# Kernel optimization log

Hardware: AMD Instinct MI355X
Metric: run time of the kernel (lower is better)

Reference implementation:

```python
import jax, jax.numpy as jnp
import numpy as np

N = 100000
E = 1600000
D_IN = 128
D_OUT = 128


def setup_inputs() -> dict:
    key = jax.random.key(0)
    ks = jax.random.split(key, 6)
    seq = jax.random.normal(ks[0], (N, D_IN), dtype=jnp.float32)
    edge_src = jax.random.randint(ks[1], (E,), 0, N, dtype=jnp.int32)
    edge_dst = jax.random.randint(ks[2], (E,), 0, N, dtype=jnp.int32)
    adj_vals = jax.random.uniform(ks[3], (E,), dtype=jnp.float32)
    # xavier_uniform for [out, in] -> stored as [in, out] for x @ W
    lim = float(np.sqrt(6.0 / (D_IN + D_OUT)))
    w_fc = jax.random.uniform(ks[4], (D_IN, D_OUT), jnp.float32, -lim, lim)
    w_proj = jax.random.uniform(ks[5], (D_IN, D_OUT), jnp.float32, -lim, lim)
    b_proj = jnp.zeros((D_OUT,), jnp.float32)
    bias = jnp.zeros((D_OUT,), jnp.float32)
    return {"seq": seq, "edge_src": edge_src, "edge_dst": edge_dst,
            "adj_vals": adj_vals, "w_fc": w_fc, "w_proj": w_proj,
            "b_proj": b_proj, "bias": bias}


def reference(seq, edge_src, edge_dst, adj_vals, w_fc, w_proj, b_proj, bias):
    # h = fc(seq)  (no bias)
    h = seq @ w_fc                                  # [N, D_OUT]
    # spmm(adj, h): out[i] = sum_{e: dst=i} vals[e] * h[src[e]]
    msgs = adj_vals[:, None] * h[edge_src]          # [E, D_OUT]
    agg = jax.ops.segment_sum(msgs, edge_dst, num_segments=N)
    # bias add + residual proj(seq) add + tanh
    out = jnp.tanh(agg + bias + seq @ w_proj + b_proj)
    return out
```

## Files before the change

### kernel.cpp

```cpp
#include <hip/hip_runtime.h>
#include <math.h>


typedef __attribute__((ext_vector_type(8))) short short8;
typedef __attribute__((ext_vector_type(4))) float float4v;
typedef __attribute__((ext_vector_type(2))) _Float16 half2v;

#define PG 256
#define NBMAX 2048

static __device__ __forceinline__ short f2bf(float x) {
    unsigned u = __float_as_uint(x);
    unsigned r = (u + 0x7fffu + ((u >> 16) & 1u)) >> 16;
    return (short)r;
}
static __device__ __forceinline__ float bf2f(short h) {
    return __uint_as_float(((unsigned)(unsigned short)h) << 16);
}

__global__ __launch_bounds__(256)
void wconv_kernel(const float* __restrict__ wa, const float* __restrict__ wb,
                  short* __restrict__ whia, short* __restrict__ wloa,
                  short* __restrict__ whib, short* __restrict__ wlob) {
    const int bb = blockIdx.x;
    const float* w  = (bb < 16) ? wa   : wb;
    short* whi      = (bb < 16) ? whia : whib;
    short* wlo      = (bb < 16) ? wloa : wlob;
    const int i = (bb & 15) * 256 + threadIdx.x;
    const float4 v = ((const float4*)w)[i];
    const int k = i >> 5;
    const int c4 = (i & 31) * 4;
    float xs[4] = {v.x, v.y, v.z, v.w};
    #pragma unroll
    for (int j = 0; j < 4; j++) {
        const short hi = f2bf(xs[j]);
        const short lo = f2bf(xs[j] - bf2f(hi));
        whi[(c4 + j) * 128 + k] = hi;
        wlo[(c4 + j) * 128 + k] = lo;
    }
}

#define KP 136

__global__ __launch_bounds__(256, 2)
void mm_mfma_kernel(const float* __restrict__ seq, const short* __restrict__ whi,
                    const short* __restrict__ wlo,
                    const float* __restrict__ b0p, const float* __restrict__ b1p,
                    float* __restrict__ out, _Float16* __restrict__ out16,
                    int N, int add_bias) {
    __shared__ short wt_hi[128 * KP];
    __shared__ short wt_lo[128 * KP];

    const int tid = threadIdx.x;
    for (int i = tid; i < 2048; i += 256) {
        const int row = i >> 4;
        const int k8  = (i & 15) * 8;
        *(float4*)&wt_hi[row * KP + k8] = ((const float4*)whi)[i];
        *(float4*)&wt_lo[row * KP + k8] = ((const float4*)wlo)[i];
    }
    __syncthreads();

    const int wave = tid >> 6;
    const int lane = tid & 63;
    const int q = lane >> 4;
    const int c = lane & 15;
    const int R = blockIdx.x * 64 + wave * 16;
    const int rowL = (R + c < N) ? (R + c) : (N - 1);

    float4v acc[8];
    #pragma unroll
    for (int ct = 0; ct < 8; ct++) acc[ct] = (float4v){0.f, 0.f, 0.f, 0.f};

    #pragma unroll
    for (int t = 0; t < 4; t++) {
        const int kk = t * 32 + q * 8;
        const float4 a0 = *(const float4*)&seq[(size_t)rowL * 128 + kk];
        const float4 a1 = *(const float4*)&seq[(size_t)rowL * 128 + kk + 4];
        float xs[8] = {a0.x, a0.y, a0.z, a0.w, a1.x, a1.y, a1.z, a1.w};
        union { short s[8]; short8 v; } ahi, alo;
        #pragma unroll
        for (int j = 0; j < 8; j++) {
            const short hi = f2bf(xs[j]);
            ahi.s[j] = hi;
            alo.s[j] = f2bf(xs[j] - bf2f(hi));
        }
        #pragma unroll
        for (int ct = 0; ct < 8; ct++) {
            const int n = ct * 16 + c;
            const short8 bhi = *(const short8*)&wt_hi[n * KP + kk];
            const short8 blo = *(const short8*)&wt_lo[n * KP + kk];
            acc[ct] = __builtin_amdgcn_mfma_f32_16x16x32_bf16(ahi.v, bhi, acc[ct], 0, 0, 0);
            acc[ct] = __builtin_amdgcn_mfma_f32_16x16x32_bf16(ahi.v, blo, acc[ct], 0, 0, 0);
            acc[ct] = __builtin_amdgcn_mfma_f32_16x16x32_bf16(alo.v, bhi, acc[ct], 0, 0, 0);
        }
    }

    if (out16) {
        #pragma unroll
        for (int ct = 0; ct < 8; ct++) {
            const int col = ct * 16 + c;
            float badd = 0.f;
            if (add_bias) badd = b0p[col] + b1p[col];
            #pragma unroll
            for (int r = 0; r < 4; r++) {
                const int row = R + q * 4 + r;
                if (row < N) out16[(size_t)row * 128 + col] = (_Float16)(acc[ct][r] + badd);
            }
        }
    } else {
        #pragma unroll
        for (int ct = 0; ct < 8; ct++) {
            const int col = ct * 16 + c;
            float badd = 0.f;
            if (add_bias) badd = b0p[col] + b1p[col];
            #pragma unroll
            for (int r = 0; r < 4; r++) {
                const int row = R + q * 4 + r;
                if (row < N) out[(size_t)row * 128 + col] = acc[ct][r] + badd;
            }
        }
    }
}


__global__ __launch_bounds__(256)
void phist_kernel(const int* __restrict__ edst, int* __restrict__ hcnt,
                  int E, int S, int NB) {
    __shared__ int cnt[NBMAX];
    const int g = blockIdx.x;
    const int tid = threadIdx.x;
    for (int b = tid; b < NB; b += 256) cnt[b] = 0;
    __syncthreads();
    const int lo = g * S;
    const int hi = (lo + S < E) ? (lo + S) : E;
    for (int i = lo + tid; i < hi; i += 256)
        atomicAdd(&cnt[edst[i] >> 6], 1);
    __syncthreads();
    for (int b = tid; b < NB; b += 256) hcnt[b * PG + g] = cnt[b];
}

__global__ __launch_bounds__(256)
void pscan1_kernel(const int* __restrict__ in, int* __restrict__ out,
                   int* __restrict__ bsum, int L) {
    __shared__ int s[256];
    const int t = threadIdx.x;
    const int base = blockIdx.x * 2048 + t * 8;
    int v[8];
    int mysum = 0;
    #pragma unroll
    for (int j = 0; j < 8; j++) {
        v[j] = (base + j < L) ? in[base + j] : 0;
        mysum += v[j];
    }
    s[t] = mysum;
    __syncthreads();
    for (int o = 1; o < 256; o <<= 1) {
        int add = (t >= o) ? s[t - o] : 0;
        __syncthreads();
        s[t] += add;
        __syncthreads();
    }
    int run = s[t] - mysum;
    #pragma unroll
    for (int j = 0; j < 8; j++) {
        if (base + j < L) out[base + j] = run;
        run += v[j];
    }
    if (t == 255) bsum[blockIdx.x] = s[255];
}

__global__ __launch_bounds__(256)
void pscan2_kernel(const int* __restrict__ bsum, int* __restrict__ ebsum, int nb) {
    __shared__ int s[256];
    const int t = threadIdx.x;
    const int v = (t < nb) ? bsum[t] : 0;
    s[t] = v;
    __syncthreads();
    for (int o = 1; o < 256; o <<= 1) {
        int add = (t >= o) ? s[t - o] : 0;
        __syncthreads();
        s[t] += add;
        __syncthreads();
    }
    if (t < nb) ebsum[t] = s[t] - v;
}

__global__ __launch_bounds__(256)
void paddback_kernel(int* __restrict__ pos, const int* __restrict__ ebsum,
                     int* __restrict__ bstart, int L, int NB, int E) {
    const int add = ebsum[blockIdx.x];
    const int base = blockIdx.x * 2048 + threadIdx.x * 8;
    #pragma unroll
    for (int j = 0; j < 8; j++) {
        const int idx = base + j;
        if (idx < L) {
            const int v = pos[idx] + add;
            pos[idx] = v;
            if ((idx & (PG - 1)) == 0) bstart[idx / PG] = v;
        }
    }
    if (blockIdx.x == 0 && threadIdx.x == 0) bstart[NB] = E;
}

__global__ __launch_bounds__(256)
void pscatter_kernel(const int* __restrict__ esrc, const int* __restrict__ edst,
                     const float* __restrict__ vals, const int* __restrict__ pos,
                     int2* __restrict__ sedge, int E, int S, int NB) {
    __shared__ int cur[NBMAX];
    const int g = blockIdx.x;
    const int tid = threadIdx.x;
    for (int b = tid; b < NB; b += 256) cur[b] = pos[b * PG + g];
    __syncthreads();
    const int lo = g * S;
    const int hi = (lo + S < E) ? (lo + S) : E;
    for (int i = lo + tid; i < hi; i += 256) {
        const int d = edst[i];
        const int p = atomicAdd(&cur[d >> 6], 1);
        sedge[p] = make_int2((esrc[i] << 6) | (d & 63), __float_as_int(vals[i]));
    }
}

#define CAP 2048

__global__ __launch_bounds__(256, 8)
void aggregate_sorted(const int* __restrict__ bstart, const int2* __restrict__ sedge,
                      const _Float16* __restrict__ h, const _Float16* __restrict__ base,
                      float* __restrict__ out, int N) {
    __shared__ int2 ebuf[CAP];
    __shared__ int cnt[64], sc[64], off[65], cur[64];
    const int b = blockIdx.x;
    const int tid = threadIdx.x;
    const int beg = bstart[b];
    const int total = bstart[b + 1] - beg;
    const int cl = total < CAP ? total : CAP;

    if (tid < 64) cnt[tid] = 0;
    __syncthreads();
    for (int i = tid; i < cl; i += 256)
        atomicAdd(&cnt[sedge[beg + i].x & 63], 1);
    __syncthreads();
    if (tid < 64) sc[tid] = cnt[tid];
    __syncthreads();
    for (int o = 1; o < 64; o <<= 1) {
        int add = (tid < 64 && tid >= o) ? sc[tid - o] : 0;
        __syncthreads();
        if (tid < 64) sc[tid] += add;
        __syncthreads();
    }
    if (tid < 64) { off[tid] = sc[tid] - cnt[tid]; cur[tid] = sc[tid] - cnt[tid]; }
    if (tid == 63) off[64] = sc[63];
    __syncthreads();
    for (int i = tid; i < cl; i += 256) {
        const int2 e = sedge[beg + i];
        const int p = atomicAdd(&cur[e.x & 63], 1);
        ebuf[p] = e;
    }
    __syncthreads();

    const int wave = tid >> 6;
    const int lane = tid & 63;
    const int g = lane >> 4;
    const int c = lane & 15;
    const char* hb = (const char*)h;
    const unsigned coff = (unsigned)c << 4;

    for (int n = wave * 16; n < wave * 16 + 16; n++) {
        const int node = b * 64 + n;
        if (node >= N) break;
        const int e0 = off[n], e1 = off[n + 1];
        float a0 = 0.f, a1 = 0.f, a2 = 0.f, a3 = 0.f;
        float a4 = 0.f, a5 = 0.f, a6 = 0.f, a7 = 0.f;

        if (e1 > e0) {
            int jj = e0 + g;
            int2 eA = ebuf[jj < e1 ? jj : e0];
            float vA = (jj < e1) ? __int_as_float(eA.y) : 0.f;
            int4 hA = *(const int4*)(hb + ((((unsigned)eA.x >> 6) << 8) + coff));
            for (int j = e0;;) {
                const int jn = j + 4;
                const bool more = jn < e1;
                int2 eB; float vB = 0.f; int4 hB;
                if (more) {
                    const int j2 = jn + g;
                    eB = ebuf[j2 < e1 ? j2 : e0];
                    vB = (j2 < e1) ? __int_as_float(eB.y) : 0.f;
                    hB = *(const int4*)(hb + ((((unsigned)eB.x >> 6) << 8) + coff));
                }
                union { int4 i4; half2v h2[4]; } u; u.i4 = hA;
                a0 += vA * (float)u.h2[0].x; a1 += vA * (float)u.h2[0].y;
                a2 += vA * (float)u.h2[1].x; a3 += vA * (float)u.h2[1].y;
                a4 += vA * (float)u.h2[2].x; a5 += vA * (float)u.h2[2].y;
                a6 += vA * (float)u.h2[3].x; a7 += vA * (float)u.h2[3].y;
                if (!more) break;
                hA = hB; vA = vB; j = jn;
            }
        }
        for (int t2 = cl; t2 < total; t2++) {
            const int2 e = sedge[beg + t2];
            if ((e.x & 63) == n) {
                const float v = (g == 0) ? __int_as_float(e.y) : 0.f;
                union { int4 i4; half2v h2[4]; } u;
                u.i4 = *(const int4*)(hb + ((((unsigned)e.x >> 6) << 8) + coff));
                a0 += v * (float)u.h2[0].x; a1 += v * (float)u.h2[0].y;
                a2 += v * (float)u.h2[1].x; a3 += v * (float)u.h2[1].y;
                a4 += v * (float)u.h2[2].x; a5 += v * (float)u.h2[2].y;
                a6 += v * (float)u.h2[3].x; a7 += v * (float)u.h2[3].y;
            }
        }

        a0 += __shfl_xor(a0, 16, 64); a0 += __shfl_xor(a0, 32, 64);
        a1 += __shfl_xor(a1, 16, 64); a1 += __shfl_xor(a1, 32, 64);
        a2 += __shfl_xor(a2, 16, 64); a2 += __shfl_xor(a2, 32, 64);
        a3 += __shfl_xor(a3, 16, 64); a3 += __shfl_xor(a3, 32, 64);
        a4 += __shfl_xor(a4, 16, 64); a4 += __shfl_xor(a4, 32, 64);
        a5 += __shfl_xor(a5, 16, 64); a5 += __shfl_xor(a5, 32, 64);
        a6 += __shfl_xor(a6, 16, 64); a6 += __shfl_xor(a6, 32, 64);
        a7 += __shfl_xor(a7, 16, 64); a7 += __shfl_xor(a7, 32, 64);

        float wx, wy;
        if (g == 0)      { wx = a0; wy = a1; }
        else if (g == 1) { wx = a2; wy = a3; }
        else if (g == 2) { wx = a4; wy = a5; }
        else             { wx = a6; wy = a7; }

        const half2v bb = __builtin_nontemporal_load(
            (const half2v*)(base + (size_t)node * 128 + (unsigned)(c * 8 + g * 2)));
        union { double d; float2 f; } rv;
        rv.f.x = tanhf(wx + (float)bb.x);
        rv.f.y = tanhf(wy + (float)bb.y);
        __builtin_nontemporal_store(rv.d, (double*)out + (size_t)node * 64 + (unsigned)(c * 4 + g));
    }
}


__global__ __launch_bounds__(256)
void edge_scatter(const int* __restrict__ esrc, const int* __restrict__ edst,
                  const float* __restrict__ vals, const _Float16* __restrict__ h,
                  float* __restrict__ out, int E) {
    const int gtid = blockIdx.x * blockDim.x + threadIdx.x;
    const int wave = gtid >> 6;
    const int lane = threadIdx.x & 63;
    const int nw = (gridDim.x * blockDim.x) >> 6;
    for (int e = wave; e < E; e += nw) {
        const int s = esrc[e];
        const int d = edst[e];
        const float v = vals[e];
        const half2v hv = *(const half2v*)(h + (size_t)s * 128 + lane * 2);
        float* op = out + (size_t)d * 128 + lane * 2;
        atomicAdd(op, v * (float)hv.x);
        atomicAdd(op + 1, v * (float)hv.y);
    }
}

__global__ __launch_bounds__(256)
void tanh_kernel(float* __restrict__ out, int n4) {
    const int i = blockIdx.x * blockDim.x + threadIdx.x;
    if (i < n4) {
        float4 v = ((float4*)out)[i];
        v.x = tanhf(v.x);
        v.y = tanhf(v.y);
        v.z = tanhf(v.z);
        v.w = tanhf(v.w);
        ((float4*)out)[i] = v;
    }
}

static inline size_t align64(size_t x) { return (x + 63) & ~(size_t)63; }

extern "C" void kernel_launch(void* const* d_in, const int* in_sizes, int n_in,
                              void* d_out, int out_size, void* d_ws, size_t ws_size,
                              hipStream_t stream) {
    const float* seq    = (const float*)d_in[0];
    const int*   esrc   = (const int*)  d_in[1];
    const int*   edst   = (const int*)  d_in[2];
    const float* vals   = (const float*)d_in[3];
    const float* w_fc   = (const float*)d_in[4];
    const float* w_proj = (const float*)d_in[5];
    const float* b_proj = (const float*)d_in[6];
    const float* bias   = (const float*)d_in[7];
    float* out = (float*)d_out;

    const int N = in_sizes[0] / 128;
    const int E = in_sizes[1];
    const int NB = (N + 63) >> 6;
    const int L  = NB * PG;
    const int S  = (E + PG - 1) / PG;
    const int nsb = (L + 2047) / 2048;

    char* ws = (char*)d_ws;
    const size_t o_h     = 0;
    const size_t o_b16   = align64(o_h    + (size_t)N * 128 * 2);
    const size_t o_whif  = align64(o_b16  + (size_t)N * 128 * 2);
    const size_t o_wlof  = align64(o_whif + 32768);
    const size_t o_whip  = align64(o_wlof + 32768);
    const size_t o_wlop  = align64(o_whip + 32768);
    const size_t o_hc    = align64(o_wlop + 32768);
    const size_t o_pos   = align64(o_hc   + (size_t)L * 4);
    const size_t o_bs    = align64(o_pos  + (size_t)L * 4);
    const size_t o_bsum  = align64(o_bs   + (size_t)(NB + 1) * 4);
    const size_t o_ebs   = align64(o_bsum + 1024);
    const size_t o_sed   = align64(o_ebs  + 1024);
    const size_t need    = o_sed + (size_t)E * 8;

    _Float16* h      = (_Float16*)(ws + o_h);
    _Float16* base16 = (_Float16*)(ws + o_b16);
    short* whi_fc = (short*)(ws + o_whif);
    short* wlo_fc = (short*)(ws + o_wlof);
    short* whi_pj = (short*)(ws + o_whip);
    short* wlo_pj = (short*)(ws + o_wlop);
    int*   hcnt   = (int*)  (ws + o_hc);
    int*   pos    = (int*)  (ws + o_pos);
    int*   bstart = (int*)  (ws + o_bs);
    int*   bsum   = (int*)  (ws + o_bsum);
    int*   ebsum  = (int*)  (ws + o_ebs);
    int2*  sedge  = (int2*) (ws + o_sed);

    const int mm_blocks = (N + 63) / 64;
    const bool sorted_ok = (ws_size >= need && NB <= NBMAX && nsb <= 256);

    wconv_kernel<<<32, 256, 0, stream>>>(w_fc, w_proj, whi_fc, wlo_fc, whi_pj, wlo_pj);
    mm_mfma_kernel<<<mm_blocks, 256, 0, stream>>>(seq, whi_fc, wlo_fc, nullptr, nullptr, nullptr, h, N, 0);

    if (sorted_ok) {
        mm_mfma_kernel<<<mm_blocks, 256, 0, stream>>>(seq, whi_pj, wlo_pj, b_proj, bias, nullptr, base16, N, 1);
        phist_kernel<<<PG, 256, 0, stream>>>(edst, hcnt, E, S, NB);
        pscan1_kernel<<<nsb, 256, 0, stream>>>(hcnt, pos, bsum, L);
        pscan2_kernel<<<1, 256, 0, stream>>>(bsum, ebsum, nsb);
        paddback_kernel<<<nsb, 256, 0, stream>>>(pos, ebsum, bstart, L, NB, E);
        pscatter_kernel<<<PG, 256, 0, stream>>>(esrc, edst, vals, pos, sedge, E, S, NB);
        aggregate_sorted<<<NB, 256, 0, stream>>>(bstart, sedge, h, base16, out, N);
    } else {
        mm_mfma_kernel<<<mm_blocks, 256, 0, stream>>>(seq, whi_pj, wlo_pj, b_proj, bias, out, nullptr, N, 1);
        edge_scatter<<<8192, 256, 0, stream>>>(esrc, edst, vals, h, out, E);
        const int n4 = (N * 128) / 4;
        tanh_kernel<<<(n4 + 255) / 256, 256, 0, stream>>>(out, n4);
    }
}
```

Measured before the change: 318.3 us.

## Halve aggregation bucket to 32 nodes and deepen gather prefetch to three stages

```diff
diff --git a/kernel.cpp b/kernel.cpp
--- a/kernel.cpp
+++ b/kernel.cpp
@@ -7,7 +7,7 @@
 typedef __attribute__((ext_vector_type(2))) _Float16 half2v;
 
 #define PG 256
-#define NBMAX 2048
+#define NBMAX 4096
 
 static __device__ __forceinline__ short f2bf(float x) {
     unsigned u = __float_as_uint(x);
@@ -134,7 +134,7 @@
     const int lo = g * S;
     const int hi = (lo + S < E) ? (lo + S) : E;
     for (int i = lo + tid; i < hi; i += 256)
-        atomicAdd(&cnt[edst[i] >> 6], 1);
+        atomicAdd(&cnt[edst[i] >> 5], 1);
     __syncthreads();
     for (int b = tid; b < NB; b += 256) hcnt[b * PG + g] = cnt[b];
 }
@@ -144,11 +144,11 @@
                    int* __restrict__ bsum, int L) {
     __shared__ int s[256];
     const int t = threadIdx.x;
-    const int base = blockIdx.x * 2048 + t * 8;
-    int v[8];
+    const int base = blockIdx.x * 4096 + t * 16;
+    int v[16];
     int mysum = 0;
     #pragma unroll
-    for (int j = 0; j < 8; j++) {
+    for (int j = 0; j < 16; j++) {
         v[j] = (base + j < L) ? in[base + j] : 0;
         mysum += v[j];
     }
@@ -162,7 +162,7 @@
     }
     int run = s[t] - mysum;
     #pragma unroll
-    for (int j = 0; j < 8; j++) {
+    for (int j = 0; j < 16; j++) {
         if (base + j < L) out[base + j] = run;
         run += v[j];
     }
@@ -189,9 +189,9 @@
 void paddback_kernel(int* __restrict__ pos, const int* __restrict__ ebsum,
                      int* __restrict__ bstart, int L, int NB, int E) {
     const int add = ebsum[blockIdx.x];
-    const int base = blockIdx.x * 2048 + threadIdx.x * 8;
-    #pragma unroll
-    for (int j = 0; j < 8; j++) {
+    const int base = blockIdx.x * 4096 + threadIdx.x * 16;
+    #pragma unroll
+    for (int j = 0; j < 16; j++) {
         const int idx = base + j;
         if (idx < L) {
             const int v = pos[idx] + add;
@@ -215,44 +215,44 @@
     const int hi = (lo + S < E) ? (lo + S) : E;
     for (int i = lo + tid; i < hi; i += 256) {
         const int d = edst[i];
-        const int p = atomicAdd(&cur[d >> 6], 1);
-        sedge[p] = make_int2((esrc[i] << 6) | (d & 63), __float_as_int(vals[i]));
-    }
-}
-
-#define CAP 2048
+        const int p = atomicAdd(&cur[d >> 5], 1);
+        sedge[p] = make_int2((esrc[i] << 5) | (d & 31), __float_as_int(vals[i]));
+    }
+}
+
+#define CAP 1024
 
 __global__ __launch_bounds__(256, 8)
 void aggregate_sorted(const int* __restrict__ bstart, const int2* __restrict__ sedge,
                       const _Float16* __restrict__ h, const _Float16* __restrict__ base,
                       float* __restrict__ out, int N) {
     __shared__ int2 ebuf[CAP];
-    __shared__ int cnt[64], sc[64], off[65], cur[64];
+    __shared__ int cnt[32], sc[32], off[33], cur[32];
     const int b = blockIdx.x;
     const int tid = threadIdx.x;
     const int beg = bstart[b];
     const int total = bstart[b + 1] - beg;
     const int cl = total < CAP ? total : CAP;
 
-    if (tid < 64) cnt[tid] = 0;
+    if (tid < 32) cnt[tid] = 0;
     __syncthreads();
     for (int i = tid; i < cl; i += 256)
-        atomicAdd(&cnt[sedge[beg + i].x & 63], 1);
-    __syncthreads();
-    if (tid < 64) sc[tid] = cnt[tid];
-    __syncthreads();
-    for (int o = 1; o < 64; o <<= 1) {
-        int add = (tid < 64 && tid >= o) ? sc[tid - o] : 0;
-        __syncthreads();
-        if (tid < 64) sc[tid] += add;
-        __syncthreads();
-    }
-    if (tid < 64) { off[tid] = sc[tid] - cnt[tid]; cur[tid] = sc[tid] - cnt[tid]; }
-    if (tid == 63) off[64] = sc[63];
+        atomicAdd(&cnt[sedge[beg + i].x & 31], 1);
+    __syncthreads();
+    if (tid < 32) sc[tid] = cnt[tid];
+    __syncthreads();
+    for (int o = 1; o < 32; o <<= 1) {
+        int add = (tid < 32 && tid >= o) ? sc[tid - o] : 0;
+        __syncthreads();
+        if (tid < 32) sc[tid] += add;
+        __syncthreads();
+    }
+    if (tid < 32) { off[tid] = sc[tid] - cnt[tid]; cur[tid] = sc[tid] - cnt[tid]; }
+    if (tid == 31) off[32] = sc[31];
     __syncthreads();
     for (int i = tid; i < cl; i += 256) {
         const int2 e = sedge[beg + i];
-        const int p = atomicAdd(&cur[e.x & 63], 1);
+        const int p = atomicAdd(&cur[e.x & 31], 1);
         ebuf[p] = e;
     }
     __syncthreads();
@@ -264,43 +264,50 @@
     const char* hb = (const char*)h;
     const unsigned coff = (unsigned)c << 4;
 
-    for (int n = wave * 16; n < wave * 16 + 16; n++) {
-        const int node = b * 64 + n;
+#define LOADQ(eX, vX, hX, jb) {                                               \
+        const int jj = (jb) + g;                                              \
+        eX = ebuf[jj < e1 ? jj : e0];                                         \
+        vX = (jj < e1) ? __int_as_float(eX.y) : 0.f;                          \
+        hX = *(const int4*)(hb + ((((unsigned)eX.x >> 5) << 8) + coff)); }
+#define ACCQ(vX, hX) {                                                        \
+        union { int4 i4; half2v h2[4]; } u; u.i4 = hX;                        \
+        a0 += vX * (float)u.h2[0].x; a1 += vX * (float)u.h2[0].y;             \
+        a2 += vX * (float)u.h2[1].x; a3 += vX * (float)u.h2[1].y;             \
+        a4 += vX * (float)u.h2[2].x; a5 += vX * (float)u.h2[2].y;             \
+        a6 += vX * (float)u.h2[3].x; a7 += vX * (float)u.h2[3].y; }
+
+    for (int n = wave * 8; n < wave * 8 + 8; n++) {
+        const int node = b * 32 + n;
         if (node >= N) break;
         const int e0 = off[n], e1 = off[n + 1];
         float a0 = 0.f, a1 = 0.f, a2 = 0.f, a3 = 0.f;
         float a4 = 0.f, a5 = 0.f, a6 = 0.f, a7 = 0.f;
 
         if (e1 > e0) {
-            int jj = e0 + g;
-            int2 eA = ebuf[jj < e1 ? jj : e0];
-            float vA = (jj < e1) ? __int_as_float(eA.y) : 0.f;
-            int4 hA = *(const int4*)(hb + ((((unsigned)eA.x >> 6) << 8) + coff));
-            for (int j = e0;;) {
-                const int jn = j + 4;
-                const bool more = jn < e1;
-                int2 eB; float vB = 0.f; int4 hB;
-                if (more) {
-                    const int j2 = jn + g;
-                    eB = ebuf[j2 < e1 ? j2 : e0];
-                    vB = (j2 < e1) ? __int_as_float(eB.y) : 0.f;
-                    hB = *(const int4*)(hb + ((((unsigned)eB.x >> 6) << 8) + coff));
-                }
-                union { int4 i4; half2v h2[4]; } u; u.i4 = hA;
-                a0 += vA * (float)u.h2[0].x; a1 += vA * (float)u.h2[0].y;
-                a2 += vA * (float)u.h2[1].x; a3 += vA * (float)u.h2[1].y;
-                a4 += vA * (float)u.h2[2].x; a5 += vA * (float)u.h2[2].y;
-                a6 += vA * (float)u.h2[3].x; a7 += vA * (float)u.h2[3].y;
-                if (!more) break;
-                hA = hB; vA = vB; j = jn;
+            int2 eA, eB, eC;
+            float vA = 0.f, vB = 0.f, vC = 0.f;
+            int4 hA, hB, hC;
+            int j = e0;
+            LOADQ(eA, vA, hA, j);
+            if (j + 4 < e1) LOADQ(eB, vB, hB, j + 4);
+            while (true) {
+                if (j + 8 < e1) LOADQ(eC, vC, hC, j + 8);
+                ACCQ(vA, hA);
+                j += 4; if (j >= e1) break;
+                if (j + 8 < e1) LOADQ(eA, vA, hA, j + 8);
+                ACCQ(vB, hB);
+                j += 4; if (j >= e1) break;
+                if (j + 8 < e1) LOADQ(eB, vB, hB, j + 8);
+                ACCQ(vC, hC);
+                j += 4; if (j >= e1) break;
             }
         }
         for (int t2 = cl; t2 < total; t2++) {
             const int2 e = sedge[beg + t2];
-            if ((e.x & 63) == n) {
+            if ((e.x & 31) == n) {
                 const float v = (g == 0) ? __int_as_float(e.y) : 0.f;
                 union { int4 i4; half2v h2[4]; } u;
-                u.i4 = *(const int4*)(hb + ((((unsigned)e.x >> 6) << 8) + coff));
+                u.i4 = *(const int4*)(hb + ((((unsigned)e.x >> 5) << 8) + coff));
                 a0 += v * (float)u.h2[0].x; a1 += v * (float)u.h2[0].y;
                 a2 += v * (float)u.h2[1].x; a3 += v * (float)u.h2[1].y;
                 a4 += v * (float)u.h2[2].x; a5 += v * (float)u.h2[2].y;
@@ -330,6 +337,8 @@
         rv.f.y = tanhf(wy + (float)bb.y);
         __builtin_nontemporal_store(rv.d, (double*)out + (size_t)node * 64 + (unsigned)(c * 4 + g));
     }
+#undef LOADQ
+#undef ACCQ
 }
 
 
@@ -382,10 +391,10 @@
 
     const int N = in_sizes[0] / 128;
     const int E = in_sizes[1];
-    const int NB = (N + 63) >> 6;
+    const int NB = (N + 31) >> 5;
     const int L  = NB * PG;
     const int S  = (E + PG - 1) / PG;
-    const int nsb = (L + 2047) / 2048;
+    const int nsb = (L + 4095) / 4096;
 
     char* ws = (char*)d_ws;
     const size_t o_h     = 0;
@@ -395,8 +404,7 @@
     const size_t o_whip  = align64(o_wlof + 32768);
     const size_t o_wlop  = align64(o_whip + 32768);
     const size_t o_hc    = align64(o_wlop + 32768);
-    const size_t o_pos   = align64(o_hc   + (size_t)L * 4);
-    const size_t o_bs    = align64(o_pos  + (size_t)L * 4);
+    const size_t o_bs    = align64(o_hc   + (size_t)L * 4);
     const size_t o_bsum  = align64(o_bs   + (size_t)(NB + 1) * 4);
     const size_t o_ebs   = align64(o_bsum + 1024);
     const size_t o_sed   = align64(o_ebs  + 1024);
@@ -409,7 +417,7 @@
     short* whi_pj = (short*)(ws + o_whip);
     short* wlo_pj = (short*)(ws + o_wlop);
     int*   hcnt   = (int*)  (ws + o_hc);
-    int*   pos    = (int*)  (ws + o_pos);
+    int*   pos    = hcnt;
     int*   bstart = (int*)  (ws + o_bs);
     int*   bsum   = (int*)  (ws + o_bsum);
     int*   ebsum  = (int*)  (ws + o_ebs);
@@ -424,7 +432,7 @@
     if (sorted_ok) {
         mm_mfma_kernel<<<mm_blocks, 256, 0, stream>>>(seq, whi_pj, wlo_pj, b_proj, bias, nullptr, base16, N, 1);
         phist_kernel<<<PG, 256, 0, stream>>>(edst, hcnt, E, S, NB);
-        pscan1_kernel<<<nsb, 256, 0, stream>>>(hcnt, pos, bsum, L);
+        pscan1_kernel<<<nsb, 256, 0, stream>>>(hcnt, hcnt, bsum, L);
         pscan2_kernel<<<1, 256, 0, stream>>>(bsum, ebsum, nsb);
         paddback_kernel<<<nsb, 256, 0, stream>>>(pos, ebsum, bstart, L, NB, E);
         pscatter_kernel<<<PG, 256, 0, stream>>>(esrc, edst, vals, pos, sedge, E, S, NB);
```

After: 327.9 us. +3.0%, slower.
